# Optimization experiments

Hardware: AMD Instinct MI355X
Metric: run time of the kernel (lower is better)

The kernel has to match this reference:

```python
import jax, jax.numpy as jnp
import numpy as np

N, E, DIM, H = 100000, 1600000, 128, 8
HD = DIM // H  # head_dim


def setup_inputs() -> dict:
    key = jax.random.key(0)
    ks = jax.random.split(key, 12)
    s = lambda k, sh, fan: jax.random.normal(k, sh, jnp.float32) * (1.0 / np.sqrt(fan))
    return {
        "x": jax.random.normal(ks[0], (N, DIM), jnp.float32),
        "src": jax.random.randint(ks[1], (E,), 0, N, jnp.int32),
        "dst": jax.random.randint(ks[2], (E,), 0, N, jnp.int32),
        # input_linear: dim -> dim
        "w_in": s(ks[3], (DIM, DIM), DIM), "b_in": jnp.zeros((DIM,), jnp.float32),
        # attn_linear_u: dim -> H (with bias); attn_linear_v: dim -> H (no bias)
        "w_au": s(ks[4], (DIM, H), DIM), "b_au": jnp.zeros((H,), jnp.float32),
        "w_av": s(ks[5], (DIM, H), DIM),
        # feed-forward: dim -> dim (hidden_dim_multiplier=1) -> dim
        "w1": s(ks[6], (DIM, DIM), DIM), "b1": jnp.zeros((DIM,), jnp.float32),
        "w2": s(ks[7], (DIM, DIM), DIM), "b2": jnpp if False else jnp.zeros((DIM,), jnp.float32),
    }


def reference(x, src, dst, w_in, b_in, w_au, b_au, w_av, w1, b1, w2, b2):
    n = x.shape[0]
    h = x @ w_in + b_in                      # [N, dim]
    a_u = h @ w_au + b_au                    # [N, H]
    a_v = h @ w_av                           # [N, H]
    # u_add_v: per-edge scores, then LeakyReLU(0.2)
    scores = jax.nn.leaky_relu(a_u[src] + a_v[dst], negative_slope=0.2)  # [E, H]
    # edge_softmax: normalize over incoming edges of each dst node
    smax = jax.ops.segment_max(scores, dst, num_segments=n)              # [N, H]
    ex = jnp.exp(scores - smax[dst])                                     # [E, H]
    denom = jax.ops.segment_sum(ex, dst, num_segments=n)                 # [N, H]
    probs = ex / denom[dst]                                              # [E, H]
    # u_mul_e_sum with x reshaped to [N, head_dim, H]
    hv = h.reshape(n, HD, H)
    msg = hv[src] * probs[:, None, :]                                    # [E, HD, H]
    agg = jax.ops.segment_sum(msg, dst, num_segments=n)                  # [N, HD, H]
    out = agg.reshape(n, DIM)
    # feed-forward (dropout=0, eval)
    out = jax.nn.gelu(out @ w1 + b1) @ w2 + b2
    return out
```

## Files before the change

kernel.cpp:

```cpp
#include <hip/hip_runtime.h>
#include <hip/hip_bf16.h>
#include <stdint.h>

#define DIM 128
#define NH 8
#define CH 4096
#define BK 128
#define LS 136
#define EBUF 4096

using bf16 = __hip_bfloat16;
typedef __attribute__((ext_vector_type(8))) short short8;
typedef __attribute__((ext_vector_type(4))) float floatx4;


__device__ inline float bf2f(unsigned short b) {
    return __uint_as_float(((unsigned)b) << 16);
}
__device__ inline unsigned short f2bf(float f) {
    unsigned u = __float_as_uint(f);
    u += 0x7FFFu + ((u >> 16) & 1u);
    return (unsigned short)(u >> 16);
}

__device__ inline float gelu_tanh(float x) {
    float x3 = x * x * x;
    float u = 0.7978845608028654f * (x + 0.044715f * x3);
    float e = __expf(2.f * u);
    float t = 1.f - 2.f / (e + 1.f);
    return 0.5f * x * (1.f + t);
}

__launch_bounds__(256)
__global__ void scatter_pre_kernel(const int* __restrict__ src, const int* __restrict__ dst,
                                   int* __restrict__ lofs, unsigned* __restrict__ packed,
                                   int E, int K, int B,
                                   const float* __restrict__ w_in, const float* __restrict__ w1,
                                   const float* __restrict__ w2, const float* __restrict__ w_au,
                                   const float* __restrict__ w_av,
                                   unsigned short* __restrict__ w_in_b, unsigned short* __restrict__ w1_b,
                                   unsigned short* __restrict__ w2_b, unsigned short* __restrict__ wc_b) {
    __shared__ int hist[1024];
    __shared__ int cur[1024];
    __shared__ int wsum[4];
    const int b = blockIdx.x, tid = threadIdx.x;
    if (b < B) {
        for (int k = tid; k < 1024; k += 256) hist[k] = 0;
        __syncthreads();
        const int base = b * CH, end = min(base + CH, E);
        for (int i = base + tid; i < end; i += 256)
            atomicAdd(&hist[dst[i] >> 7], 1);
        __syncthreads();
        int v[4]; int t = 0;
        #pragma unroll
        for (int j = 0; j < 4; ++j) { int x = hist[tid * 4 + j]; v[j] = t; t += x; }
        const int lane = tid & 63, wv = tid >> 6;
        int incl = t;
        #pragma unroll
        for (int off = 1; off < 64; off <<= 1) {
            int y = __shfl_up(incl, off);
            if (lane >= off) incl += y;
        }
        if (lane == 63) wsum[wv] = incl;
        __syncthreads();
        int woff = 0;
        #pragma unroll
        for (int w = 0; w < 4; ++w) if (w < wv) woff += wsum[w];
        int texcl = woff + incl - t;
        #pragma unroll
        for (int j = 0; j < 4; ++j) {
            int k = tid * 4 + j;
            int e = texcl + v[j];
            cur[k] = e;
            if (k < K) lofs[(size_t)b * K + k] = e;
        }
        __syncthreads();
        for (int i = base + tid; i < end; i += 256) {
            int d = dst[i], s = src[i];
            int pos = atomicAdd(&cur[d >> 7], 1);
            packed[(size_t)b * CH + pos] = (unsigned)s | ((unsigned)(d & 127) << 20);
        }
    } else {
        int pb = b - B;
        if (pb < 12) {
            const int m = pb >> 2, qtr = pb & 3;
            const float* W = m == 0 ? w_in : (m == 1 ? w1 : w2);
            unsigned short* O = m == 0 ? w_in_b : (m == 1 ? w1_b : w2_b);
            const bool perm = (m == 1);
            #pragma unroll
            for (int i = 0; i < 16; ++i) {
                int o = qtr * 4096 + tid + i * 256;
                int k = o & 127, n = o >> 7;
                int krow = perm ? ((k & 15) * 8 + (k >> 4)) : k;
                O[o] = f2bf(W[krow * 128 + n]);
            }
        } else {
            #pragma unroll
            for (int i = 0; i < 8; ++i) {
                int o = tid + i * 256;
                int j = o >> 7, kt = o & 127;
                int ko = (kt & 15) * 8 + (kt >> 4);
                float v = (j < 8) ? w_au[ko * 8 + j] : w_av[ko * 8 + (j - 8)];
                wc_b[o] = f2bf(v);
            }
        }
    }
}

__device__ __forceinline__ void stage_pre(unsigned short* wt, const unsigned short* __restrict__ pre,
                                          int tid) {
    #pragma unroll
    for (int i = 0; i < 4; ++i) {
        int g = tid + i * 512;
        short8 v = *(const short8*)(pre + g * 8);
        *(short8*)(wt + (g >> 4) * LS + (g & 15) * 8) = v;
    }
}

__launch_bounds__(512)
__global__ void gemm_in_attn_kernel(const float* __restrict__ x, const unsigned short* __restrict__ w_in_b,
                                    const float* __restrict__ b_in,
                                    const unsigned short* __restrict__ wc_b, const float* __restrict__ b_au,
                                    bf16* __restrict__ h, float* __restrict__ au,
                                    float* __restrict__ av, int M) {
    __shared__ __align__(16) unsigned short wt[128 * LS];
    __shared__ __align__(16) unsigned short wc[16 * LS];
    const int tid = threadIdx.x;

    stage_pre(wt, w_in_b, tid);
    {
        int j = tid >> 5, kt4 = (tid & 31) * 4;
        const unsigned* s = (const unsigned*)(wc_b + j * 128 + kt4);
        unsigned* d = (unsigned*)(wc + j * LS + kt4);
        d[0] = s[0]; d[1] = s[1];
    }
    __syncthreads();

    const int wave = tid >> 6;
    const int lane = tid & 63;
    const int l15 = lane & 15;
    const int q = lane >> 4;
    const int rowbase = blockIdx.x * 128 + wave * 16;
    const int rowA = min(rowbase + l15, M - 1);

    floatx4 acc[8];
    #pragma unroll
    for (int c = 0; c < 8; ++c) acc[c] = (floatx4){0.f, 0.f, 0.f, 0.f};

    #pragma unroll
    for (int kk = 0; kk < 4; ++kk) {
        const float* ap = x + (size_t)rowA * 128 + kk * 32 + q * 8;
        floatx4 a0 = *(const floatx4*)ap;
        floatx4 a1 = *(const floatx4*)(ap + 4);
        union { short8 s; unsigned short u[8]; } cv;
        #pragma unroll
        for (int j = 0; j < 4; ++j) { cv.u[j] = f2bf(a0[j]); cv.u[4 + j] = f2bf(a1[j]); }
        short8 afrag = cv.s;
        #pragma unroll
        for (int c = 0; c < 8; ++c) {
            short8 bfrag = *(const short8*)(wt + (c * 16 + l15) * LS + kk * 32 + q * 8);
            acc[c] = __builtin_amdgcn_mfma_f32_16x16x32_bf16(afrag, bfrag, acc[c], 0, 0, 0);
        }
    }
    __syncthreads();

    const int rl0 = wave * 16 + q * 4;
    #pragma unroll
    for (int c = 0; c < 8; ++c) {
        int col = c * 16 + l15;
        int colw = (col & 7) * 16 + (col >> 3);
        float b = b_in[col];
        #pragma unroll
        for (int r = 0; r < 4; ++r)
            wt[(rl0 + r) * LS + colw] = f2bf(acc[c][r] + b);
    }
    __syncthreads();

    const int blk0 = blockIdx.x * 128;
    #pragma unroll
    for (int i = 0; i < 4; ++i) {
        int g = tid + i * 512;
        int row = g >> 4;
        if (blk0 + row < M) {
            short8 v = *(const short8*)(wt + row * LS + (g & 15) * 8);
            *(short8*)((unsigned short*)h + (size_t)(blk0 + row) * 128 + (g & 15) * 8) = v;
        }
    }

    floatx4 acc2 = (floatx4){0.f, 0.f, 0.f, 0.f};
    #pragma unroll
    for (int kk = 0; kk < 4; ++kk) {
        short8 af = *(const short8*)(wt + (wave * 16 + l15) * LS + kk * 32 + q * 8);
        short8 bf = *(const short8*)(wc + l15 * LS + kk * 32 + q * 8);
        acc2 = __builtin_amdgcn_mfma_f32_16x16x32_bf16(af, bf, acc2, 0, 0, 0);
    }
    {
        const int row0 = rowbase + q * 4;
        int col = l15;
        #pragma unroll
        for (int r = 0; r < 4; ++r) {
            int rr = row0 + r;
            if (rr < M) {
                if (col < 8) au[(size_t)rr * 8 + col] = acc2[r] + b_au[col];
                else         av[(size_t)rr * 8 + (col - 8)] = acc2[r];
            }
        }
    }
}

__launch_bounds__(512)
__global__ void ff_kernel(const bf16* __restrict__ A, const unsigned short* __restrict__ w1_b,
                          const float* __restrict__ b1, const unsigned short* __restrict__ w2_b,
                          const float* __restrict__ b2, float* __restrict__ out, int M) {
    __shared__ __align__(16) unsigned short wt[128 * LS];
    __shared__ __align__(16) unsigned short ht[128 * LS];
    const int tid = threadIdx.x;

    stage_pre(wt, w1_b, tid);
    __syncthreads();

    const int wave = tid >> 6;
    const int lane = tid & 63;
    const int l15 = lane & 15;
    const int q = lane >> 4;
    const int rowbase = blockIdx.x * 128 + wave * 16;
    const int rowA = min(rowbase + l15, M - 1);

    floatx4 acc[8];
    #pragma unroll
    for (int c = 0; c < 8; ++c) acc[c] = (floatx4){0.f, 0.f, 0.f, 0.f};

    #pragma unroll
    for (int kk = 0; kk < 4; ++kk) {
        short8 afrag = *(const short8*)((const unsigned short*)A + (size_t)rowA * 128 + kk * 32 + q * 8);
        #pragma unroll
        for (int c = 0; c < 8; ++c) {
            short8 bfrag = *(const short8*)(wt + (c * 16 + l15) * LS + kk * 32 + q * 8);
            acc[c] = __builtin_amdgcn_mfma_f32_16x16x32_bf16(afrag, bfrag, acc[c], 0, 0, 0);
        }
    }
    __syncthreads();

    stage_pre(wt, w2_b, tid);
    const int rl0 = wave * 16 + q * 4;
    #pragma unroll
    for (int c = 0; c < 8; ++c) {
        int col = c * 16 + l15;
        float b = b1[col];
        #pragma unroll
        for (int r = 0; r < 4; ++r)
            ht[(rl0 + r) * LS + col] = f2bf(gelu_tanh(acc[c][r] + b));
    }
    __syncthreads();

    floatx4 acc2[8];
    #pragma unroll
    for (int c = 0; c < 8; ++c) acc2[c] = (floatx4){0.f, 0.f, 0.f, 0.f};
    #pragma unroll
    for (int kk = 0; kk < 4; ++kk) {
        short8 af = *(const short8*)(ht + (wave * 16 + l15) * LS + kk * 32 + q * 8);
        #pragma unroll
        for (int c = 0; c < 8; ++c) {
            short8 bfrag = *(const short8*)(wt + (c * 16 + l15) * LS + kk * 32 + q * 8);
            acc2[c] = __builtin_amdgcn_mfma_f32_16x16x32_bf16(af, bfrag, acc2[c], 0, 0, 0);
        }
    }

    const int row0 = rowbase + q * 4;
    #pragma unroll
    for (int c = 0; c < 8; ++c) {
        int col = c * 16 + l15;
        float b = b2[col];
        #pragma unroll
        for (int r = 0; r < 4; ++r) {
            int rr = row0 + r;
            if (rr < M) out[(size_t)rr * 128 + col] = acc2[c][r] + b;
        }
    }
}


__device__ __forceinline__ void unpack8fma(uint4 w, float p, float* o) {
    o[0] = fmaf(p, __uint_as_float(w.x << 16), o[0]);
    o[1] = fmaf(p, __uint_as_float(w.x & 0xFFFF0000u), o[1]);
    o[2] = fmaf(p, __uint_as_float(w.y << 16), o[2]);
    o[3] = fmaf(p, __uint_as_float(w.y & 0xFFFF0000u), o[3]);
    o[4] = fmaf(p, __uint_as_float(w.z << 16), o[4]);
    o[5] = fmaf(p, __uint_as_float(w.z & 0xFFFF0000u), o[5]);
    o[6] = fmaf(p, __uint_as_float(w.w << 16), o[6]);
    o[7] = fmaf(p, __uint_as_float(w.w & 0xFFFF0000u), o[7]);
}

template <bool MASKED>
__device__ __forceinline__ void do8e_lds(const unsigned* ep, int i, int nd,
                                         int e, int head, int d0b,
                                         const float* __restrict__ au,
                                         const char* __restrict__ hpb,
                                         float avh, float& l, float* o) {
    int idx = i + e;
    int s;
    float m = 1.f;
    if constexpr (MASKED) {
        s = (int)ep[min(idx, nd - 1)];
        m = idx < nd ? 1.f : 0.f;
    } else {
        s = (int)ep[idx];
    }
    float a = au[(s << 3) + head];
    size_t off = ((size_t)(unsigned)s) << 8;
    uint4 w0 = *(const uint4*)(hpb + off + d0b);
    uint4 w1 = *(const uint4*)(hpb + off + d0b + 16);
    float x = a + avh;
    x = fmaxf(x, 0.2f * x);
    float p = __expf(x);
    if constexpr (MASKED) p *= m;
    l += p;
    unpack8fma(w0, p, o);
    unpack8fma(w1, p, o + 8);
}

__launch_bounds__(512)
__global__ void csr_agg_kernel(const unsigned* __restrict__ packed, const int* __restrict__ lofs,
                               const float* __restrict__ au, const float* __restrict__ av,
                               const bf16* __restrict__ h, bf16* __restrict__ agg,
                               int N, int E, int K, int B) {
    __shared__ unsigned ebuf[EBUF];
    __shared__ unsigned ebuf2[EBUF];
    __shared__ int dsc[512];
    __shared__ int hist[128], cur[128], rpl[128];
    __shared__ int wsum[8];
    __shared__ int wtot;
    const int k = blockIdx.x, tid = threadIdx.x;
    const int lane = tid & 63, wv = tid >> 6;

    int lo = 0, hi = 0;
    if (tid < B) {
        lo = lofs[(size_t)tid * K + k];
        int chunk_len = min(CH, E - tid * CH);
        hi = (k + 1 < K) ? lofs[(size_t)tid * K + (k + 1)] : chunk_len;
    }
    int len = hi - lo;
    if (tid < 128) hist[tid] = 0;
    int incl = len;
    #pragma unroll
    for (int off = 1; off < 64; off <<= 1) {
        int y = __shfl_up(incl, off);
        if (lane >= off) incl += y;
    }
    if (lane == 63) wsum[wv] = incl;
    __syncthreads();
    int woff = 0, cnt = 0;
    #pragma unroll
    for (int w = 0; w < 8; ++w) { int s = wsum[w]; if (w < wv) woff += s; cnt += s; }
    if (tid < B) dsc[tid] = woff + incl - len;
    __syncthreads();

    for (int b = tid; b < B; b += 512) {
        int blo = lofs[(size_t)b * K + k];
        int chunk_len = min(CH, E - b * CH);
        int bhi = (k + 1 < K) ? lofs[(size_t)b * K + (k + 1)] : chunk_len;
        int dbase = dsc[b];
        const unsigned* sp = packed + (size_t)b * CH;
        for (int j = blo; j < bhi; ++j) ebuf[dbase + (j - blo)] = sp[j];
    }
    __syncthreads();

    for (int i = tid; i < cnt; i += 512)
        atomicAdd(&hist[ebuf[i] >> 20], 1);
    __syncthreads();

    int v = (tid < 128) ? hist[tid] : 0;
    int incl2 = v;
    #pragma unroll
    for (int off = 1; off < 64; off <<= 1) {
        int y = __shfl_up(incl2, off);
        if (lane >= off) incl2 += y;
    }
    if (tid == 63) wtot = incl2;
    __syncthreads();
    int excl = incl2 - v + ((tid >= 64 && tid < 128) ? wtot : 0);
    if (tid < 128) { rpl[tid] = excl; cur[tid] = excl; }
    __syncthreads();

    for (int i = tid; i < cnt; i += 512) {
        unsigned p = ebuf[i];
        int pos = atomicAdd(&cur[p >> 20], 1);
        ebuf2[pos] = p & 0xFFFFFu;
    }
    __syncthreads();

    const int e = lane >> 3;
    const int head = lane & 7;
    const int d0b = head * 32;
    const char* hpb = (const char*)h;

    for (int t = 0; t < 16; ++t) {
        int nl = wv * 16 + t;
        int node = k * BK + nl;
        if (node >= N) break;
        const int nd = hist[nl];
        const unsigned* ep = ebuf2 + rpl[nl];
        const float avh = av[((size_t)node << 3) + head];

        float l0 = 0.f;
        float o[16];
        #pragma unroll
        for (int j = 0; j < 16; ++j) o[j] = 0.f;

        int i = 0;
        for (; i + 16 <= nd; i += 16) {
            do8e_lds<false>(ep, i, nd, e, head, d0b, au, hpb, avh, l0, o);
            do8e_lds<false>(ep, i + 8, nd, e, head, d0b, au, hpb, avh, l0, o);
        }
        if (i + 8 <= nd) { do8e_lds<false>(ep, i, nd, e, head, d0b, au, hpb, avh, l0, o); i += 8; }
        if (i < nd) do8e_lds<true>(ep, i, nd, e, head, d0b, au, hpb, avh, l0, o);

        #pragma unroll
        for (int j = 0; j < 16; ++j) {
            o[j] += __shfl_xor(o[j], 8);
            o[j] += __shfl_xor(o[j], 16);
            o[j] += __shfl_xor(o[j], 32);
        }
        l0 += __shfl_xor(l0, 8);
        l0 += __shfl_xor(l0, 16);
        l0 += __shfl_xor(l0, 32);

        if (lane < 8) {
            float inv = l0 > 0.f ? 1.f / l0 : 0.f;
            unsigned r[8];
            #pragma unroll
            for (int j = 0; j < 8; ++j)
                r[j] = ((unsigned)f2bf(o[2 * j + 1] * inv) << 16) | (unsigned)f2bf(o[2 * j] * inv);
            char* outp = (char*)agg + ((size_t)node << 8) + lane * 32;
            *(uint4*)outp = (uint4){r[0], r[1], r[2], r[3]};
            *(uint4*)(outp + 16) = (uint4){r[4], r[5], r[6], r[7]};
        }
    }
}

extern "C" void kernel_launch(void* const* d_in, const int* in_sizes, int n_in,
                              void* d_out, int out_size, void* d_ws, size_t ws_size,
                              hipStream_t stream) {
    const float* x    = (const float*)d_in[0];
    const int*   src  = (const int*)d_in[1];
    const int*   dst  = (const int*)d_in[2];
    const float* w_in = (const float*)d_in[3];
    const float* b_in = (const float*)d_in[4];
    const float* w_au = (const float*)d_in[5];
    const float* b_au = (const float*)d_in[6];
    const float* w_av = (const float*)d_in[7];
    const float* w1   = (const float*)d_in[8];
    const float* b1   = (const float*)d_in[9];
    const float* w2   = (const float*)d_in[10];
    const float* b2   = (const float*)d_in[11];
    const int N = in_sizes[0] / DIM;
    const int E = in_sizes[1];
    const int K = (N + BK - 1) / BK;
    const int B = (E + CH - 1) / CH;

    char* p = (char*)d_ws;
    bf16* h      = (bf16*)p; p += (size_t)N * DIM * 2;
    float* au    = (float*)p; p += (size_t)N * NH * 4;
    float* av    = (float*)p; p += (size_t)N * NH * 4;
    bf16* agg    = (bf16*)p; p += (size_t)N * DIM * 2;
    unsigned* packed = (unsigned*)p; p += (size_t)B * CH * 4;
    int* lofs  = (int*)p; p += (size_t)B * K * 4;
    unsigned short* w_in_b = (unsigned short*)p; p += 128 * 128 * 2;
    unsigned short* w1_b   = (unsigned short*)p; p += 128 * 128 * 2;
    unsigned short* w2_b   = (unsigned short*)p; p += 128 * 128 * 2;
    unsigned short* wc_b   = (unsigned short*)p; p += 16 * 128 * 2;

    const int row_blocks = (N + 127) / 128;

    scatter_pre_kernel<<<B + 13, 256, 0, stream>>>(src, dst, lofs, packed,
                                                   E, K, B, w_in, w1, w2, w_au, w_av,
                                                   w_in_b, w1_b, w2_b, wc_b);

    gemm_in_attn_kernel<<<row_blocks, 512, 0, stream>>>(x, w_in_b, b_in, wc_b, b_au,
                                                        h, au, av, N);

    csr_agg_kernel<<<K, 512, 0, stream>>>(packed, lofs, au, av, h, agg, N, E, K, B);

    ff_kernel<<<row_blocks, 512, 0, stream>>>(agg, w1_b, b1, w2_b, b2, (float*)d_out, N);
}
```

Baseline: 285.2 us.

## Build global CSR alongside input GEMM, aggregate with one wave per node

The per-bucket edge sort (gather packed edges, histogram, local scatter) now runs as extra blocks inside the input GEMM/attention-logit kernel, so it can overlap with the GEMM. It writes a global CSR (rowptr, deg, esrc) with buckets placed by an atomic counter. The aggregation kernel becomes a lightweight one-wave-per-node kernel that reads sources from global memory instead of LDS. This gives finer load balance and overlaps the sort, at the cost of an extra global write and read of the edge list. The packed/lofs buffers are aliased onto agg to save workspace.

```diff
diff --git a/kernel.cpp b/kernel.cpp
--- a/kernel.cpp
+++ b/kernel.cpp
@@ -8,6 +8,7 @@
 #define BK 128
 #define LS 136
 #define EBUF 4096
+#define SMEM_BYTES 39936
 
 using bf16 = __hip_bfloat16;
 typedef __attribute__((ext_vector_type(8))) short short8;
@@ -34,7 +35,7 @@
 __launch_bounds__(256)
 __global__ void scatter_pre_kernel(const int* __restrict__ src, const int* __restrict__ dst,
                                    int* __restrict__ lofs, unsigned* __restrict__ packed,
-                                   int E, int K, int B,
+                                   int* __restrict__ total, int E, int K, int B,
                                    const float* __restrict__ w_in, const float* __restrict__ w1,
                                    const float* __restrict__ w2, const float* __restrict__ w_au,
                                    const float* __restrict__ w_av,
@@ -103,6 +104,7 @@
                 float v = (j < 8) ? w_au[ko * 8 + j] : w_av[ko * 8 + (j - 8)];
                 wc_b[o] = f2bf(v);
             }
+            if (tid == 0) total[0] = 0;
         }
     }
 }
@@ -118,14 +120,97 @@
 }
 
 __launch_bounds__(512)
-__global__ void gemm_in_attn_kernel(const float* __restrict__ x, const unsigned short* __restrict__ w_in_b,
-                                    const float* __restrict__ b_in,
-                                    const unsigned short* __restrict__ wc_b, const float* __restrict__ b_au,
-                                    bf16* __restrict__ h, float* __restrict__ au,
-                                    float* __restrict__ av, int M) {
-    __shared__ __align__(16) unsigned short wt[128 * LS];
-    __shared__ __align__(16) unsigned short wc[16 * LS];
+__global__ void gia_bcsr_kernel(const float* __restrict__ x, const unsigned short* __restrict__ w_in_b,
+                                const float* __restrict__ b_in,
+                                const unsigned short* __restrict__ wc_b, const float* __restrict__ b_au,
+                                bf16* __restrict__ h, float* __restrict__ au,
+                                float* __restrict__ av, int M, int RB,
+                                const unsigned* __restrict__ packed, const int* __restrict__ lofs,
+                                int* __restrict__ total, int* __restrict__ rowptr,
+                                int* __restrict__ deg, int* __restrict__ esrc,
+                                int N, int E, int K, int B) {
+    __shared__ __align__(16) char smem[SMEM_BYTES];
     const int tid = threadIdx.x;
+    const int lane = tid & 63, wv = tid >> 6;
+
+    if ((int)blockIdx.x >= RB) {
+        unsigned* ebuf  = (unsigned*)smem;
+        unsigned* ebuf2 = ebuf + EBUF;
+        int* dsc  = (int*)(ebuf2 + EBUF);
+        int* hist = dsc + 512;
+        int* cur  = hist + 128;
+        int* rpl  = cur + 128;
+        int* wsum = rpl + 128;
+        int* scal = wsum + 8;
+        const int k = blockIdx.x - RB;
+
+        int lo = 0, hi = 0;
+        if (tid < B) {
+            lo = lofs[(size_t)tid * K + k];
+            int chunk_len = min(CH, E - tid * CH);
+            hi = (k + 1 < K) ? lofs[(size_t)tid * K + (k + 1)] : chunk_len;
+        }
+        int len = hi - lo;
+        if (tid < 128) hist[tid] = 0;
+        int incl = len;
+        #pragma unroll
+        for (int off = 1; off < 64; off <<= 1) {
+            int y = __shfl_up(incl, off);
+            if (lane >= off) incl += y;
+        }
+        if (lane == 63) wsum[wv] = incl;
+        __syncthreads();
+        int woff = 0, cnt = 0;
+        #pragma unroll
+        for (int w = 0; w < 8; ++w) { int s = wsum[w]; if (w < wv) woff += s; cnt += s; }
+        if (tid < B) dsc[tid] = woff + incl - len;
+        if (tid == 0) scal[1] = atomicAdd(total, cnt);
+        __syncthreads();
+        const int start = scal[1];
+
+        for (int b = tid; b < B; b += 512) {
+            int blo = lofs[(size_t)b * K + k];
+            int chunk_len = min(CH, E - b * CH);
+            int bhi = (k + 1 < K) ? lofs[(size_t)b * K + (k + 1)] : chunk_len;
+            int dbase = dsc[b];
+            const unsigned* sp = packed + (size_t)b * CH;
+            for (int j = blo; j < bhi; ++j) ebuf[dbase + (j - blo)] = sp[j];
+        }
+        __syncthreads();
+
+        for (int i = tid; i < cnt; i += 512)
+            atomicAdd(&hist[ebuf[i] >> 20], 1);
+        __syncthreads();
+        int v = (tid < 128) ? hist[tid] : 0;
+        int incl2 = v;
+        #pragma unroll
+        for (int off = 1; off < 64; off <<= 1) {
+            int y = __shfl_up(incl2, off);
+            if (lane >= off) incl2 += y;
+        }
+        if (tid == 63) scal[0] = incl2;
+        __syncthreads();
+        int excl = incl2 - v + ((tid >= 64 && tid < 128) ? scal[0] : 0);
+        if (tid < 128) { rpl[tid] = excl; cur[tid] = excl; }
+        __syncthreads();
+
+        for (int i = tid; i < cnt; i += 512) {
+            unsigned p = ebuf[i];
+            int pos = atomicAdd(&cur[p >> 20], 1);
+            ebuf2[pos] = p & 0xFFFFFu;
+        }
+        __syncthreads();
+
+        for (int i = tid; i < cnt; i += 512) esrc[start + i] = (int)ebuf2[i];
+        if (tid < 128) {
+            int n = k * BK + tid;
+            if (n < N) { rowptr[n] = start + rpl[tid]; deg[n] = hist[tid]; }
+        }
+        return;
+    }
+
+    unsigned short* wt = (unsigned short*)smem;
+    unsigned short* wc = (unsigned short*)(smem + 34816);
 
     stage_pre(wt, w_in_b, tid);
     {
@@ -136,11 +221,9 @@
     }
     __syncthreads();
 
-    const int wave = tid >> 6;
-    const int lane = tid & 63;
     const int l15 = lane & 15;
     const int q = lane >> 4;
-    const int rowbase = blockIdx.x * 128 + wave * 16;
+    const int rowbase = blockIdx.x * 128 + wv * 16;
     const int rowA = min(rowbase + l15, M - 1);
 
     floatx4 acc[8];
@@ -164,7 +247,7 @@
     }
     __syncthreads();
 
-    const int rl0 = wave * 16 + q * 4;
+    const int rl0 = wv * 16 + q * 4;
     #pragma unroll
     for (int c = 0; c < 8; ++c) {
         int col = c * 16 + l15;
@@ -190,7 +273,7 @@
     floatx4 acc2 = (floatx4){0.f, 0.f, 0.f, 0.f};
     #pragma unroll
     for (int kk = 0; kk < 4; ++kk) {
-        short8 af = *(const short8*)(wt + (wave * 16 + l15) * LS + kk * 32 + q * 8);
+        short8 af = *(const short8*)(wt + (wv * 16 + l15) * LS + kk * 32 + q * 8);
         short8 bf = *(const short8*)(wc + l15 * LS + kk * 32 + q * 8);
         acc2 = __builtin_amdgcn_mfma_f32_16x16x32_bf16(af, bf, acc2, 0, 0, 0);
     }
@@ -292,19 +375,19 @@
 }
 
 template <bool MASKED>
-__device__ __forceinline__ void do8e_lds(const unsigned* ep, int i, int nd,
-                                         int e, int head, int d0b,
-                                         const float* __restrict__ au,
-                                         const char* __restrict__ hpb,
-                                         float avh, float& l, float* o) {
+__device__ __forceinline__ void do8e(const int* __restrict__ ep, int i, int nd,
+                                     int e, int head, int d0b,
+                                     const float* __restrict__ au,
+                                     const char* __restrict__ hpb,
+                                     float avh, float& l, float* o) {
     int idx = i + e;
     int s;
     float m = 1.f;
     if constexpr (MASKED) {
-        s = (int)ep[min(idx, nd - 1)];
+        s = ep[min(idx, nd - 1)];
         m = idx < nd ? 1.f : 0.f;
     } else {
-        s = (int)ep[idx];
+        s = ep[idx];
     }
     float a = au[(s << 3) + head];
     size_t off = ((size_t)(unsigned)s) << 8;
@@ -319,122 +402,55 @@
     unpack8fma(w1, p, o + 8);
 }
 
-__launch_bounds__(512)
-__global__ void csr_agg_kernel(const unsigned* __restrict__ packed, const int* __restrict__ lofs,
+__launch_bounds__(256)
+__global__ void agg_csr_kernel(const int* __restrict__ rowptr, const int* __restrict__ deg,
+                               const int* __restrict__ esrc,
                                const float* __restrict__ au, const float* __restrict__ av,
-                               const bf16* __restrict__ h, bf16* __restrict__ agg,
-                               int N, int E, int K, int B) {
-    __shared__ unsigned ebuf[EBUF];
-    __shared__ unsigned ebuf2[EBUF];
-    __shared__ int dsc[512];
-    __shared__ int hist[128], cur[128], rpl[128];
-    __shared__ int wsum[8];
-    __shared__ int wtot;
-    const int k = blockIdx.x, tid = threadIdx.x;
-    const int lane = tid & 63, wv = tid >> 6;
-
-    int lo = 0, hi = 0;
-    if (tid < B) {
-        lo = lofs[(size_t)tid * K + k];
-        int chunk_len = min(CH, E - tid * CH);
-        hi = (k + 1 < K) ? lofs[(size_t)tid * K + (k + 1)] : chunk_len;
-    }
-    int len = hi - lo;
-    if (tid < 128) hist[tid] = 0;
-    int incl = len;
-    #pragma unroll
-    for (int off = 1; off < 64; off <<= 1) {
-        int y = __shfl_up(incl, off);
-        if (lane >= off) incl += y;
-    }
-    if (lane == 63) wsum[wv] = incl;
-    __syncthreads();
-    int woff = 0, cnt = 0;
-    #pragma unroll
-    for (int w = 0; w < 8; ++w) { int s = wsum[w]; if (w < wv) woff += s; cnt += s; }
-    if (tid < B) dsc[tid] = woff + incl - len;
-    __syncthreads();
-
-    for (int b = tid; b < B; b += 512) {
-        int blo = lofs[(size_t)b * K + k];
-        int chunk_len = min(CH, E - b * CH);
-        int bhi = (k + 1 < K) ? lofs[(size_t)b * K + (k + 1)] : chunk_len;
-        int dbase = dsc[b];
-        const unsigned* sp = packed + (size_t)b * CH;
-        for (int j = blo; j < bhi; ++j) ebuf[dbase + (j - blo)] = sp[j];
-    }
-    __syncthreads();
-
-    for (int i = tid; i < cnt; i += 512)
-        atomicAdd(&hist[ebuf[i] >> 20], 1);
-    __syncthreads();
-
-    int v = (tid < 128) ? hist[tid] : 0;
-    int incl2 = v;
-    #pragma unroll
-    for (int off = 1; off < 64; off <<= 1) {
-        int y = __shfl_up(incl2, off);
-        if (lane >= off) incl2 += y;
-    }
-    if (tid == 63) wtot = incl2;
-    __syncthreads();
-    int excl = incl2 - v + ((tid >= 64 && tid < 128) ? wtot : 0);
-    if (tid < 128) { rpl[tid] = excl; cur[tid] = excl; }
-    __syncthreads();
-
-    for (int i = tid; i < cnt; i += 512) {
-        unsigned p = ebuf[i];
-        int pos = atomicAdd(&cur[p >> 20], 1);
-        ebuf2[pos] = p & 0xFFFFFu;
-    }
-    __syncthreads();
-
+                               const bf16* __restrict__ h, bf16* __restrict__ agg, int N) {
+    const int node = (blockIdx.x * 256 + threadIdx.x) >> 6;
+    if (node >= N) return;
+    const int lane = threadIdx.x & 63;
     const int e = lane >> 3;
     const int head = lane & 7;
     const int d0b = head * 32;
     const char* hpb = (const char*)h;
-
-    for (int t = 0; t < 16; ++t) {
-        int nl = wv * 16 + t;
-        int node = k * BK + nl;
-        if (node >= N) break;
-        const int nd = hist[nl];
-        const unsigned* ep = ebuf2 + rpl[nl];
-        const float avh = av[((size_t)node << 3) + head];
-
-        float l0 = 0.f;
-        float o[16];
-        #pragma unroll
-        for (int j = 0; j < 16; ++j) o[j] = 0.f;
-
-        int i = 0;
-        for (; i + 16 <= nd; i += 16) {
-            do8e_lds<false>(ep, i, nd, e, head, d0b, au, hpb, avh, l0, o);
-            do8e_lds<false>(ep, i + 8, nd, e, head, d0b, au, hpb, avh, l0, o);
-        }
-        if (i + 8 <= nd) { do8e_lds<false>(ep, i, nd, e, head, d0b, au, hpb, avh, l0, o); i += 8; }
-        if (i < nd) do8e_lds<true>(ep, i, nd, e, head, d0b, au, hpb, avh, l0, o);
-
-        #pragma unroll
-        for (int j = 0; j < 16; ++j) {
-            o[j] += __shfl_xor(o[j], 8);
-            o[j] += __shfl_xor(o[j], 16);
-            o[j] += __shfl_xor(o[j], 32);
-        }
-        l0 += __shfl_xor(l0, 8);
-        l0 += __shfl_xor(l0, 16);
-        l0 += __shfl_xor(l0, 32);
-
-        if (lane < 8) {
-            float inv = l0 > 0.f ? 1.f / l0 : 0.f;
-            unsigned r[8];
-            #pragma unroll
-            for (int j = 0; j < 8; ++j)
-                r[j] = ((unsigned)f2bf(o[2 * j + 1] * inv) << 16) | (unsigned)f2bf(o[2 * j] * inv);
-            char* outp = (char*)agg + ((size_t)node << 8) + lane * 32;
-            *(uint4*)outp = (uint4){r[0], r[1], r[2], r[3]};
-            *(uint4*)(outp + 16) = (uint4){r[4], r[5], r[6], r[7]};
-        }
+    const int nd = deg[node];
+    const int start = rowptr[node];
+    const float avh = av[((size_t)node << 3) + head];
+    const int* ep = esrc + start;
+
+    float l0 = 0.f;
+    float o[16];
+    #pragma unroll
+    for (int j = 0; j < 16; ++j) o[j] = 0.f;
+
+    int i = 0;
+    for (; i + 16 <= nd; i += 16) {
+        do8e<false>(ep, i, nd, e, head, d0b, au, hpb, avh, l0, o);
+        do8e<false>(ep, i + 8, nd, e, head, d0b, au, hpb, avh, l0, o);
+    }
+    if (i + 8 <= nd) { do8e<false>(ep, i, nd, e, head, d0b, au, hpb, avh, l0, o); i += 8; }
+    if (i < nd) do8e<true>(ep, i, nd, e, head, d0b, au, hpb, avh, l0, o);
+
+    #pragma unroll
+    for (int j = 0; j < 16; ++j) {
+        o[j] += __shfl_xor(o[j], 8);
+        o[j] += __shfl_xor(o[j], 16);
+        o[j] += __shfl_xor(o[j], 32);
+    }
+    l0 += __shfl_xor(l0, 8);
+    l0 += __shfl_xor(l0, 16);
+    l0 += __shfl_xor(l0, 32);
+
+    if (lane < 8) {
+        float inv = l0 > 0.f ? 1.f / l0 : 0.f;
+        unsigned r[8];
+        #pragma unroll
+        for (int j = 0; j < 8; ++j)
+            r[j] = ((unsigned)f2bf(o[2 * j + 1] * inv) << 16) | (unsigned)f2bf(o[2 * j] * inv);
+        char* outp = (char*)agg + ((size_t)node << 8) + lane * 32;
+        *(uint4*)outp = (uint4){r[0], r[1], r[2], r[3]};
+        *(uint4*)(outp + 16) = (uint4){r[4], r[5], r[6], r[7]};
     }
 }
 
@@ -459,27 +475,33 @@
     const int B = (E + CH - 1) / CH;
 
     char* p = (char*)d_ws;
+    int*  deg    = (int*)p;  p += (size_t)N * 4;
+    int*  rowptr = (int*)p;  p += (size_t)N * 4;
+    int*  esrc   = (int*)p;  p += (size_t)E * 4;
     bf16* h      = (bf16*)p; p += (size_t)N * DIM * 2;
     float* au    = (float*)p; p += (size_t)N * NH * 4;
     float* av    = (float*)p; p += (size_t)N * NH * 4;
-    bf16* agg    = (bf16*)p; p += (size_t)N * DIM * 2;
-    unsigned* packed = (unsigned*)p; p += (size_t)B * CH * 4;
-    int* lofs  = (int*)p; p += (size_t)B * K * 4;
     unsigned short* w_in_b = (unsigned short*)p; p += 128 * 128 * 2;
     unsigned short* w1_b   = (unsigned short*)p; p += 128 * 128 * 2;
     unsigned short* w2_b   = (unsigned short*)p; p += 128 * 128 * 2;
     unsigned short* wc_b   = (unsigned short*)p; p += 16 * 128 * 2;
+    int* total = (int*)p; p += 64;
+    bf16* agg    = (bf16*)p;  p += (size_t)N * DIM * 2;
+    unsigned* packed = (unsigned*)agg;
+    int* lofs  = (int*)((char*)agg + (size_t)B * CH * 4);
 
     const int row_blocks = (N + 127) / 128;
 
-    scatter_pre_kernel<<<B + 13, 256, 0, stream>>>(src, dst, lofs, packed,
+    scatter_pre_kernel<<<B + 13, 256, 0, stream>>>(src, dst, lofs, packed, total,
                                                    E, K, B, w_in, w1, w2, w_au, w_av,
                                                    w_in_b, w1_b, w2_b, wc_b);
 
-    gemm_in_attn_kernel<<<row_blocks, 512, 0, stream>>>(x, w_in_b, b_in, wc_b, b_au,
-                                                        h, au, av, N);
-
-    csr_agg_kernel<<<K, 512, 0, stream>>>(packed, lofs, au, av, h, agg, N, E, K, B);
+    gia_bcsr_kernel<<<row_blocks + K, 512, 0, stream>>>(x, w_in_b, b_in, wc_b, b_au,
+                                                        h, au, av, N, row_blocks,
+                                                        packed, lofs, total,
+                                                        rowptr, deg, esrc, N, E, K, B);
+
+    agg_csr_kernel<<<(N + 3) / 4, 256, 0, stream>>>(rowptr, deg, esrc, au, av, h, agg, N);
 
     ff_kernel<<<row_blocks, 512, 0, stream>>>(agg, w1_b, b1, w2_b, b2, (float*)d_out, N);
 }
```

Result: faster. 261.6 us (-8.2%).
